# Kernel tuning notes

Hardware: AMD Instinct MI355X
Metric: run time of the kernel (lower is better)

Reference implementation:

```python
import jax, jax.numpy as jnp
import numpy as np

K = 10
ALPHA = 0.1
N_NODES = 100000
N_EDGES = 1600000
IN_DIM = 128
HID_DIM = 128
OUT_DIM = 128


def setup_inputs() -> dict:
    key = jax.random.key(0)
    k_x, k_e, k_w1, k_b1, k_w2, k_b2 = jax.random.split(key, 6)
    x = jax.random.normal(k_x, (N_NODES, IN_DIM), dtype=jnp.float32)
    edge_index = jax.random.randint(k_e, (2, N_EDGES), 0, N_NODES, dtype=jnp.int64)
    # Linear params (Kaiming-uniform-ish scale, exact init irrelevant for correctness)
    s1 = 1.0 / np.sqrt(IN_DIM)
    s2 = 1.0 / np.sqrt(HID_DIM)
    W1 = jax.random.uniform(k_w1, (IN_DIM, HID_DIM), jnp.float32, -s1, s1)
    b1 = jax.random.uniform(k_b1, (HID_DIM,), jnp.float32, -s1, s1)
    W2 = jax.random.uniform(k_w2, (HID_DIM, OUT_DIM), jnp.float32, -s2, s2)
    b2 = jax.random.uniform(k_b2, (OUT_DIM,), jnp.float32, -s2, s2)
    return {"x": x, "edge_index": edge_index, "W1": W1, "b1": b1, "W2": W2, "b2": b2}


def reference(x, edge_index, W1, b1, W2, b2):
    n = x.shape[0]
    h = jax.nn.relu(x @ W1 + b1)  # [N, H]

    # gcn_norm: add self loops, symmetric normalization D^-1/2 (A+I) D^-1/2
    loop = jnp.arange(n, dtype=edge_index.dtype)
    src = jnp.concatenate([edge_index[0], loop])  # [E+N]
    dst = jnp.concatenate([edge_index[1], loop])  # [E+N]
    ones = jnp.ones(src.shape[0], dtype=h.dtype)
    deg = jax.ops.segment_sum(ones, dst, num_segments=n)  # [N]
    dinv = jnp.where(deg > 0, jax.lax.rsqrt(deg), 0.0)
    norm = (dinv[src] * dinv[dst])[:, None]  # [E+N, 1]

    # APPNP: K steps of h = (1-alpha) * A_hat h + alpha * h0
    h0 = h

    def step(h, _):
        msg = norm * h[src]  # gather + scale  [E+N, H]
        agg = jax.ops.segment_sum(msg, dst, num_segments=n)  # scatter-add [N, H]
        return (1.0 - ALPHA) * agg + ALPHA * h0, None

    h, _ = jax.lax.scan(step, h, None, length=K)
    return h @ W2 + b2
```

## Files before the change

### kernel.cpp

```cpp
#include <hip/hip_runtime.h>
#include <stdint.h>

#define N_NODES 100000
#define N_EDGES 1600000
#define HDIM    128
#define KSTEPS  10

typedef unsigned int uint;

#define SCAN_T     256
#define SCAN_I     4
#define SCAN_ELEMS (SCAN_T * SCAN_I)
#define SCAN_NB    ((N_NODES + SCAN_ELEMS - 1) / SCAN_ELEMS)

__device__ inline float2 bf2_to_f2(uint v) {
    float2 r;
    r.x = __uint_as_float(v << 16);
    r.y = __uint_as_float(v & 0xffff0000u);
    return r;
}
__device__ inline uint f_to_bf_bits(float f) {
    uint u = __float_as_uint(f);
    return (u + 0x7fffu + ((u >> 16) & 1u)) >> 16;
}
__device__ inline uint f2_to_bf2(float x, float y) {
    return f_to_bf_bits(x) | (f_to_bf_bits(y) << 16);
}

__global__ void k_count(const int* __restrict__ eidx, int* __restrict__ cnt) {
    int e = blockIdx.x * blockDim.x + threadIdx.x;
    if (e < N_EDGES) {
        unsigned d = (unsigned)eidx[N_EDGES + e];
        if (d < N_NODES) atomicAdd(&cnt[d], 1);
    }
}

__global__ void k_scan1(const int* __restrict__ cnt, int* __restrict__ rp,
                        int* __restrict__ bsum) {
    __shared__ int s[SCAN_T];
    int tid  = threadIdx.x;
    int base = blockIdx.x * SCAN_ELEMS + tid * SCAN_I;
    int v[SCAN_I];
    int loc = 0;
#pragma unroll
    for (int j = 0; j < SCAN_I; ++j) {
        int idx = base + j;
        v[j] = (idx < N_NODES) ? cnt[idx] : 0;
        loc += v[j];
    }
    s[tid] = loc;
    __syncthreads();
    for (int off = 1; off < SCAN_T; off <<= 1) {
        int t = (tid >= off) ? s[tid - off] : 0;
        __syncthreads();
        s[tid] += t;
        __syncthreads();
    }
    int run = s[tid] - loc;
#pragma unroll
    for (int j = 0; j < SCAN_I; ++j) {
        int idx = base + j;
        if (idx < N_NODES) rp[idx] = run;
        run += v[j];
    }
    if (tid == SCAN_T - 1) bsum[blockIdx.x] = s[SCAN_T - 1];
}

__global__ void k_scan2(const int* __restrict__ bsum, int* __restrict__ boff,
                        int* __restrict__ rp) {
    int acc = 0;
    for (int i = 0; i < SCAN_NB; ++i) { boff[i] = acc; acc += bsum[i]; }
    rp[N_NODES] = acc;
}

__global__ void k_scan3(int* __restrict__ rp, const int* __restrict__ boff) {
    int off = boff[blockIdx.x];
#pragma unroll
    for (int j = 0; j < SCAN_I; ++j) {
        int i = blockIdx.x * SCAN_ELEMS + threadIdx.x + j * SCAN_T;
        if (i < N_NODES) rp[i] += off;
    }
}

__global__ void k_dinv(const int* __restrict__ cnt, float* __restrict__ dinv,
                       float* __restrict__ dsq) {
    int i = blockIdx.x * blockDim.x + threadIdx.x;
    if (i < N_NODES) {
        float d = 1.0f + (float)cnt[i];
        dinv[i] = rsqrtf(d);
        dsq[i]  = sqrtf(d);
    }
}

__global__ void k_fill(const int* __restrict__ eidx, const int* __restrict__ rp,
                       int* __restrict__ cursor, int* __restrict__ col) {
    int e = blockIdx.x * blockDim.x + threadIdx.x;
    if (e < N_EDGES) {
        unsigned d = (unsigned)eidx[N_EDGES + e];
        unsigned s = (unsigned)eidx[e];
        if (d < N_NODES && s < N_NODES) {
            int pos = rp[d] + atomicAdd(&cursor[d], 1);
            col[pos] = (int)s;
        }
    }
}

#define KCH 64
__global__ __launch_bounds__(256)
void k_gemm1(const float* __restrict__ x, const float* __restrict__ W,
             const float* __restrict__ bias, const float* __restrict__ dinv,
             uint* __restrict__ out) {
    __shared__ __align__(16) float wlds[KCH][HDIM];
    __shared__ __align__(16) float xs[32][KCH + 1];
    int tid  = threadIdx.x;
    int tx   = tid & 31, ty = tid >> 5;
    int row0 = blockIdx.x * 32;

    float4 bc = *(const float4*)&bias[tx * 4];

    float acc[4][4] = {};
    for (int kc = 0; kc < HDIM; kc += KCH) {
#pragma unroll
        for (int i = 0; i < 8; ++i) {
            int id = tid + i * 256;
            int kk = id >> 5, n4 = id & 31;
            *(float4*)&wlds[kk][n4 * 4] =
                *(const float4*)&W[(size_t)(kc + kk) * HDIM + n4 * 4];
        }
#pragma unroll
        for (int i = 0; i < 2; ++i) {
            int id = tid + i * 256;
            int r = id >> 4, c4 = id & 15;
            float4 v = *(const float4*)&x[(size_t)(row0 + r) * HDIM + kc + c4 * 4];
            xs[r][c4 * 4 + 0] = v.x;
            xs[r][c4 * 4 + 1] = v.y;
            xs[r][c4 * 4 + 2] = v.z;
            xs[r][c4 * 4 + 3] = v.w;
        }
        __syncthreads();
#pragma unroll 8
        for (int kk = 0; kk < KCH; ++kk) {
            float4 b4 = *(const float4*)&wlds[kk][tx * 4];
            float a0 = xs[ty * 4 + 0][kk];
            float a1 = xs[ty * 4 + 1][kk];
            float a2 = xs[ty * 4 + 2][kk];
            float a3 = xs[ty * 4 + 3][kk];
            acc[0][0] += a0 * b4.x; acc[0][1] += a0 * b4.y; acc[0][2] += a0 * b4.z; acc[0][3] += a0 * b4.w;
            acc[1][0] += a1 * b4.x; acc[1][1] += a1 * b4.y; acc[1][2] += a1 * b4.z; acc[1][3] += a1 * b4.w;
            acc[2][0] += a2 * b4.x; acc[2][1] += a2 * b4.y; acc[2][2] += a2 * b4.z; acc[2][3] += a2 * b4.w;
            acc[3][0] += a3 * b4.x; acc[3][1] += a3 * b4.y; acc[3][2] += a3 * b4.z; acc[3][3] += a3 * b4.w;
        }
        __syncthreads();
    }
#pragma unroll
    for (int r = 0; r < 4; ++r) {
        int row = row0 + ty * 4 + r;
        float di = dinv[row];
        float v0 = fmaxf(acc[r][0] + bc.x, 0.0f) * di;
        float v1 = fmaxf(acc[r][1] + bc.y, 0.0f) * di;
        float v2 = fmaxf(acc[r][2] + bc.z, 0.0f) * di;
        float v3 = fmaxf(acc[r][3] + bc.w, 0.0f) * di;
        uint2 p;
        p.x = f2_to_bf2(v0, v1);
        p.y = f2_to_bf2(v2, v3);
        *(uint2*)&out[(size_t)row * 64 + tx * 2] = p;
    }
}

__global__ __launch_bounds__(256)
void k_gemm2(const uint* __restrict__ u, const float* __restrict__ W,
             const float* __restrict__ bias, const float* __restrict__ dsq,
             float* __restrict__ out) {
    __shared__ __align__(16) float wlds[KCH][HDIM];
    __shared__ __align__(16) float xs[32][KCH + 1];
    int tid  = threadIdx.x;
    int tx   = tid & 31, ty = tid >> 5;
    int row0 = blockIdx.x * 32;

    float4 bc = *(const float4*)&bias[tx * 4];

    float acc[4][4] = {};
    for (int kc = 0; kc < HDIM; kc += KCH) {
#pragma unroll
        for (int i = 0; i < 8; ++i) {
            int id = tid + i * 256;
            int kk = id >> 5, n4 = id & 31;
            *(float4*)&wlds[kk][n4 * 4] =
                *(const float4*)&W[(size_t)(kc + kk) * HDIM + n4 * 4];
        }
#pragma unroll
        for (int i = 0; i < 2; ++i) {
            int id = tid + i * 256;
            int r = id >> 4, c4 = id & 15;
            float ds = dsq[row0 + r];
            uint2 v = *(const uint2*)&u[(size_t)(row0 + r) * 64 + (kc >> 1) + c4 * 2];
            float2 f0 = bf2_to_f2(v.x);
            float2 f1 = bf2_to_f2(v.y);
            xs[r][c4 * 4 + 0] = f0.x * ds;
            xs[r][c4 * 4 + 1] = f0.y * ds;
            xs[r][c4 * 4 + 2] = f1.x * ds;
            xs[r][c4 * 4 + 3] = f1.y * ds;
        }
        __syncthreads();
#pragma unroll 8
        for (int kk = 0; kk < KCH; ++kk) {
            float4 b4 = *(const float4*)&wlds[kk][tx * 4];
            float a0 = xs[ty * 4 + 0][kk];
            float a1 = xs[ty * 4 + 1][kk];
            float a2 = xs[ty * 4 + 2][kk];
            float a3 = xs[ty * 4 + 3][kk];
            acc[0][0] += a0 * b4.x; acc[0][1] += a0 * b4.y; acc[0][2] += a0 * b4.z; acc[0][3] += a0 * b4.w;
            acc[1][0] += a1 * b4.x; acc[1][1] += a1 * b4.y; acc[1][2] += a1 * b4.z; acc[1][3] += a1 * b4.w;
            acc[2][0] += a2 * b4.x; acc[2][1] += a2 * b4.y; acc[2][2] += a2 * b4.z; acc[2][3] += a2 * b4.w;
            acc[3][0] += a3 * b4.x; acc[3][1] += a3 * b4.y; acc[3][2] += a3 * b4.z; acc[3][3] += a3 * b4.w;
        }
        __syncthreads();
    }
#pragma unroll
    for (int r = 0; r < 4; ++r) {
        int row = row0 + ty * 4 + r;
        float4 v;
        v.x = acc[r][0] + bc.x;
        v.y = acc[r][1] + bc.y;
        v.z = acc[r][2] + bc.z;
        v.w = acc[r][3] + bc.w;
        *(float4*)&out[(size_t)row * HDIM + tx * 4] = v;
    }
}

__global__ __launch_bounds__(256)
void k_step(const uint* __restrict__ uin, const uint* __restrict__ u0,
            uint* __restrict__ uout, const int* __restrict__ col,
            const int* __restrict__ rp, const float* __restrict__ dinv) {
    int wid  = (blockIdx.x * blockDim.x + threadIdx.x) >> 6;
    int node = __builtin_amdgcn_readfirstlane(wid);
    int lane = threadIdx.x & 63;
    if (node >= N_NODES) return;

    size_t self = (size_t)node * 64 + lane;
    uint usv = uin[self];
    uint uzv = __builtin_nontemporal_load(&u0[self]);
    float di = dinv[node];
    float w  = 0.9f * di * di;

    int beg = rp[node], end = rp[node + 1];
    float2 us = bf2_to_f2(usv);
    float accx = us.x, accy = us.y;

    int e = beg;
    for (; e + 8 <= end; e += 8) {
        int s0 = col[e + 0], s1 = col[e + 1], s2 = col[e + 2], s3 = col[e + 3];
        int s4 = col[e + 4], s5 = col[e + 5], s6 = col[e + 6], s7 = col[e + 7];
        uint b0 = uin[(size_t)s0 * 64 + lane];
        uint b1 = uin[(size_t)s1 * 64 + lane];
        uint b2 = uin[(size_t)s2 * 64 + lane];
        uint b3 = uin[(size_t)s3 * 64 + lane];
        uint b4 = uin[(size_t)s4 * 64 + lane];
        uint b5 = uin[(size_t)s5 * 64 + lane];
        uint b6 = uin[(size_t)s6 * 64 + lane];
        uint b7 = uin[(size_t)s7 * 64 + lane];
        float2 a0 = bf2_to_f2(b0), a1 = bf2_to_f2(b1);
        float2 a2 = bf2_to_f2(b2), a3 = bf2_to_f2(b3);
        float2 a4 = bf2_to_f2(b4), a5 = bf2_to_f2(b5);
        float2 a6 = bf2_to_f2(b6), a7 = bf2_to_f2(b7);
        accx += ((a0.x + a1.x) + (a2.x + a3.x)) + ((a4.x + a5.x) + (a6.x + a7.x));
        accy += ((a0.y + a1.y) + (a2.y + a3.y)) + ((a4.y + a5.y) + (a6.y + a7.y));
    }
    for (; e + 2 <= end; e += 2) {
        int s0 = col[e], s1 = col[e + 1];
        uint b0 = uin[(size_t)s0 * 64 + lane];
        uint b1 = uin[(size_t)s1 * 64 + lane];
        float2 a0 = bf2_to_f2(b0), a1 = bf2_to_f2(b1);
        accx += a0.x + a1.x;
        accy += a0.y + a1.y;
    }
    if (e < end) {
        uint b0 = uin[(size_t)col[e] * 64 + lane];
        float2 a0 = bf2_to_f2(b0);
        accx += a0.x;
        accy += a0.y;
    }
    float2 uz = bf2_to_f2(uzv);
    float ox = w * accx + 0.1f * uz.x;
    float oy = w * accy + 0.1f * uz.y;
    __builtin_nontemporal_store(f2_to_bf2(ox, oy), &uout[self]);
}

extern "C" void kernel_launch(void* const* d_in, const int* in_sizes, int n_in,
                              void* d_out, int out_size, void* d_ws, size_t ws_size,
                              hipStream_t stream) {
    (void)in_sizes; (void)n_in; (void)out_size; (void)ws_size;
    const float* x  = (const float*)d_in[0];
    const int*   ei = (const int*)d_in[1];
    const float* W1 = (const float*)d_in[2];
    const float* b1 = (const float*)d_in[3];
    const float* W2 = (const float*)d_in[4];
    const float* b2 = (const float*)d_in[5];
    float* out = (float*)d_out;

    char* ws = (char*)d_ws;
    size_t off = 0;
    auto alloc = [&](size_t bytes) -> void* {
        void* p = ws + off;
        off += (bytes + 255) & ~(size_t)255;
        return p;
    };
    uint*  u0   = (uint*)alloc(sizeof(uint) * (size_t)N_NODES * 64);
    uint*  uA   = (uint*)alloc(sizeof(uint) * (size_t)N_NODES * 64);
    uint*  uB   = (uint*)alloc(sizeof(uint) * (size_t)N_NODES * 64);
    int*   col  = (int*)alloc(sizeof(int) * N_EDGES);
    int*   rp   = (int*)alloc(sizeof(int) * (N_NODES + 1));
    int*   cnt  = (int*)alloc(sizeof(int) * N_NODES);
    int*   cur  = (int*)alloc(sizeof(int) * N_NODES);
    float* dinv = (float*)alloc(sizeof(float) * N_NODES);
    float* dsq  = (float*)alloc(sizeof(float) * N_NODES);
    int*   bsum = (int*)alloc(sizeof(int) * SCAN_NB);
    int*   boff = (int*)alloc(sizeof(int) * SCAN_NB);

    hipMemsetAsync(cnt, 0, sizeof(int) * N_NODES, stream);
    hipMemsetAsync(cur, 0, sizeof(int) * N_NODES, stream);

    k_count<<<N_EDGES / 256, 256, 0, stream>>>(ei, cnt);
    k_scan1<<<SCAN_NB, SCAN_T, 0, stream>>>(cnt, rp, bsum);
    k_scan2<<<1, 1, 0, stream>>>(bsum, boff, rp);
    k_scan3<<<SCAN_NB, SCAN_T, 0, stream>>>(rp, boff);
    k_dinv<<<(N_NODES + 255) / 256, 256, 0, stream>>>(cnt, dinv, dsq);
    k_fill<<<N_EDGES / 256, 256, 0, stream>>>(ei, rp, cur, col);

    k_gemm1<<<N_NODES / 32, 256, 0, stream>>>(x, W1, b1, dinv, u0);

    const uint* uin = u0;
    uint* uout = uA;
    for (int k = 0; k < KSTEPS; ++k) {
        k_step<<<N_NODES / 4, 256, 0, stream>>>(uin, u0, uout, col, rp, dinv);
        uin = uout;
        uout = (uout == uA) ? uB : uA;
    }
    k_gemm2<<<N_NODES / 32, 256, 0, stream>>>(uin, W2, b2, dsq, out);
}
```

Before: 993.5 us.

## Record edge slot positions during counting and zone-partition the CSR fill scatter

The count kernel now stores the atomicAdd return value as each edge's slot within its destination row and reads edge indices as int4. This removes the second atomic pass and the cursor array from the fill. The fill kernel becomes a 2D grid over 8 destination zones. Each block re-reads an edge chunk and writes only edges whose destination falls in its zone, which localizes scattered writes to col at the cost of reading the edge data 8 times. The step kernel's remainder loop is also unrolled into 4/2/1 tail blocks. The range checks on node indices are dropped, and the int4 loads assume N_EDGES is a multiple of 4.

```diff
diff --git a/kernel.cpp b/kernel.cpp
--- a/kernel.cpp
+++ b/kernel.cpp
@@ -5,6 +5,8 @@
 #define N_EDGES 1600000
 #define HDIM    128
 #define KSTEPS  10
+#define NZONE   8
+#define ZDIV    12500u
 
 typedef unsigned int uint;
 
@@ -27,11 +29,17 @@
     return f_to_bf_bits(x) | (f_to_bf_bits(y) << 16);
 }
 
-__global__ void k_count(const int* __restrict__ eidx, int* __restrict__ cnt) {
-    int e = blockIdx.x * blockDim.x + threadIdx.x;
-    if (e < N_EDGES) {
-        unsigned d = (unsigned)eidx[N_EDGES + e];
-        if (d < N_NODES) atomicAdd(&cnt[d], 1);
+__global__ void k_countpos(const int* __restrict__ eidx, int* __restrict__ cnt,
+                           int* __restrict__ pos) {
+    int e0 = (blockIdx.x * blockDim.x + threadIdx.x) * 4;
+    if (e0 < N_EDGES) {
+        int4 d4 = *(const int4*)&eidx[N_EDGES + e0];
+        int4 p;
+        p.x = atomicAdd(&cnt[d4.x], 1);
+        p.y = atomicAdd(&cnt[d4.y], 1);
+        p.z = atomicAdd(&cnt[d4.z], 1);
+        p.w = atomicAdd(&cnt[d4.w], 1);
+        *(int4*)&pos[e0] = p;
     }
 }
 
@@ -92,15 +100,24 @@
     }
 }
 
-__global__ void k_fill(const int* __restrict__ eidx, const int* __restrict__ rp,
-                       int* __restrict__ cursor, int* __restrict__ col) {
-    int e = blockIdx.x * blockDim.x + threadIdx.x;
-    if (e < N_EDGES) {
-        unsigned d = (unsigned)eidx[N_EDGES + e];
-        unsigned s = (unsigned)eidx[e];
-        if (d < N_NODES && s < N_NODES) {
-            int pos = rp[d] + atomicAdd(&cursor[d], 1);
-            col[pos] = (int)s;
+#define FCHUNK 8192
+#define FECH   ((N_EDGES + FCHUNK - 1) / FCHUNK)
+__global__ __launch_bounds__(256)
+void k_fill2(const int* __restrict__ eidx, const int* __restrict__ rp,
+             const int* __restrict__ pos, int* __restrict__ col) {
+    uint zone = blockIdx.x;
+    int  base = blockIdx.y * FCHUNK;
+#pragma unroll
+    for (int i = 0; i < FCHUNK / 1024; ++i) {
+        int e0 = base + (i * 256 + (int)threadIdx.x) * 4;
+        if (e0 < N_EDGES) {
+            int4 d4 = *(const int4*)&eidx[N_EDGES + e0];
+            int4 s4 = *(const int4*)&eidx[e0];
+            int4 p4 = *(const int4*)&pos[e0];
+            if ((uint)d4.x / ZDIV == zone) col[rp[d4.x] + p4.x] = s4.x;
+            if ((uint)d4.y / ZDIV == zone) col[rp[d4.y] + p4.y] = s4.y;
+            if ((uint)d4.z / ZDIV == zone) col[rp[d4.z] + p4.z] = s4.z;
+            if ((uint)d4.w / ZDIV == zone) col[rp[d4.w] + p4.w] = s4.w;
         }
     }
 }
@@ -266,13 +283,26 @@
         accx += ((a0.x + a1.x) + (a2.x + a3.x)) + ((a4.x + a5.x) + (a6.x + a7.x));
         accy += ((a0.y + a1.y) + (a2.y + a3.y)) + ((a4.y + a5.y) + (a6.y + a7.y));
     }
-    for (; e + 2 <= end; e += 2) {
+    if (e + 4 <= end) {
+        int s0 = col[e], s1 = col[e + 1], s2 = col[e + 2], s3 = col[e + 3];
+        uint b0 = uin[(size_t)s0 * 64 + lane];
+        uint b1 = uin[(size_t)s1 * 64 + lane];
+        uint b2 = uin[(size_t)s2 * 64 + lane];
+        uint b3 = uin[(size_t)s3 * 64 + lane];
+        float2 a0 = bf2_to_f2(b0), a1 = bf2_to_f2(b1);
+        float2 a2 = bf2_to_f2(b2), a3 = bf2_to_f2(b3);
+        accx += (a0.x + a1.x) + (a2.x + a3.x);
+        accy += (a0.y + a1.y) + (a2.y + a3.y);
+        e += 4;
+    }
+    if (e + 2 <= end) {
         int s0 = col[e], s1 = col[e + 1];
         uint b0 = uin[(size_t)s0 * 64 + lane];
         uint b1 = uin[(size_t)s1 * 64 + lane];
         float2 a0 = bf2_to_f2(b0), a1 = bf2_to_f2(b1);
         accx += a0.x + a1.x;
         accy += a0.y + a1.y;
+        e += 2;
     }
     if (e < end) {
         uint b0 = uin[(size_t)col[e] * 64 + lane];
@@ -309,23 +339,25 @@
     uint*  uA   = (uint*)alloc(sizeof(uint) * (size_t)N_NODES * 64);
     uint*  uB   = (uint*)alloc(sizeof(uint) * (size_t)N_NODES * 64);
     int*   col  = (int*)alloc(sizeof(int) * N_EDGES);
+    int*   pos  = (int*)alloc(sizeof(int) * N_EDGES);
     int*   rp   = (int*)alloc(sizeof(int) * (N_NODES + 1));
     int*   cnt  = (int*)alloc(sizeof(int) * N_NODES);
-    int*   cur  = (int*)alloc(sizeof(int) * N_NODES);
     float* dinv = (float*)alloc(sizeof(float) * N_NODES);
     float* dsq  = (float*)alloc(sizeof(float) * N_NODES);
     int*   bsum = (int*)alloc(sizeof(int) * SCAN_NB);
     int*   boff = (int*)alloc(sizeof(int) * SCAN_NB);
 
     hipMemsetAsync(cnt, 0, sizeof(int) * N_NODES, stream);
-    hipMemsetAsync(cur, 0, sizeof(int) * N_NODES, stream);
-
-    k_count<<<N_EDGES / 256, 256, 0, stream>>>(ei, cnt);
+
+    k_countpos<<<(N_EDGES / 4 + 255) / 256, 256, 0, stream>>>(ei, cnt, pos);
     k_scan1<<<SCAN_NB, SCAN_T, 0, stream>>>(cnt, rp, bsum);
     k_scan2<<<1, 1, 0, stream>>>(bsum, boff, rp);
     k_scan3<<<SCAN_NB, SCAN_T, 0, stream>>>(rp, boff);
     k_dinv<<<(N_NODES + 255) / 256, 256, 0, stream>>>(cnt, dinv, dsq);
-    k_fill<<<N_EDGES / 256, 256, 0, stream>>>(ei, rp, cur, col);
+    {
+        dim3 g(NZONE, FECH);
+        k_fill2<<<g, 256, 0, stream>>>(ei, rp, pos, col);
+    }
 
     k_gemm1<<<N_NODES / 32, 256, 0, stream>>>(x, W1, b1, dinv, u0);
 
```

Result: faster. 924.9 us (-6.9%).
